# Kernel tuning notes

Measured on AMD Instinct MI355X. Metric: run time of the kernel, lower is better.

Reference implementation:

```python
import jax, jax.numpy as jnp
import numpy as np

HID = 256
IN_DIM = 256
OUT_DIM = 10
L_CYCLES = 6
H_CYCLES = 3
BATCH = 131072
LN_EPS = 1e-5


def _layernorm(v, w, b):
    mu = jnp.mean(v, axis=-1, keepdims=True)
    var = jnp.mean(jnp.square(v - mu), axis=-1, keepdims=True)
    return (v - mu) * jax.lax.rsqrt(var + LN_EPS) * w + b


def setup_inputs() -> dict:
    key = jax.random.key(0)
    ks = jax.random.split(key, 12)
    s = lambda fan_in: 1.0 / np.sqrt(fan_in)
    inp = {
        "x": jax.random.normal(ks[0], (BATCH, IN_DIM), dtype=jnp.float32),
        "W_in": jax.random.uniform(ks[1], (IN_DIM, HID), jnp.float32, -s(IN_DIM), s(IN_DIM)),
        "b_in": jnp.zeros((HID,), jnp.float32),
        "y_init": jax.random.normal(ks[2], (1, HID), dtype=jnp.float32) * 0.02,
        "W_up": jax.random.uniform(ks[3], (HID, 4 * HID), jnp.float32, -s(HID), s(HID)),
        "b_up": jnp.zeros((4 * HID,), jnp.float32),
        "W_down": jax.random.uniform(ks[4], (4 * HID, HID), jnp.float32, -s(4 * HID), s(4 * HID)),
        "b_down": jnp.zeros((HID,), jnp.float32),
        "ln_w": jnp.ones((HID,), jnp.float32),
        "ln_b": jnp.zeros((HID,), jnp.float32),
        "W_comb": jax.random.uniform(ks[5], (2 * HID, HID), jnp.float32, -s(2 * HID), s(2 * HID)),
        "b_comb": jnp.zeros((HID,), jnp.float32),
        "W_yt": jax.random.uniform(ks[6], (HID, HID), jnp.float32, -s(HID), s(HID)),
        "b_yt": jnp.zeros((HID,), jnp.float32),
        "W_head": jax.random.uniform(ks[7], (HID, OUT_DIM), jnp.float32, -s(HID), s(HID)),
        "b_head": jnp.zeros((OUT_DIM,), jnp.float32),
    }
    return inp


def reference(x, W_in, b_in, y_init, W_up, b_up, W_down, b_down, ln_w, ln_b,
              W_comb, b_comb, W_yt, b_yt, W_head, b_head):
    z = x @ W_in + b_in                      # [B, H]
    y = jnp.broadcast_to(y_init, (x.shape[0], HID))
    for _ in range(H_CYCLES):
        for _ in range(L_CYCLES):
            h = jax.nn.gelu(z @ W_up + b_up, approximate=False)
            h = h @ W_down + b_down
            z = _layernorm(z + h, ln_w, ln_b)
        combined = jnp.concatenate([z, y], axis=-1)   # [B, 2H]
        h = jax.nn.gelu(combined @ W_comb + b_comb, approximate=False)
        y = y + h @ W_yt + b_yt
    return y @ W_head + b_head
```

## Files before the change

kernel.cpp:

```cpp
#include <hip/hip_runtime.h>

typedef _Float16 h16;
typedef h16 h16x8 __attribute__((ext_vector_type(8)));
typedef float f32x4 __attribute__((ext_vector_type(4)));

#define MFMA16(a, b, c) __builtin_amdgcn_mfma_f32_16x16x32_f16(a, b, c, 0, 0, 0)

typedef __attribute__((address_space(1))) const char gconst_char;
typedef __attribute__((address_space(3))) char lds_char;
#define GL_LDS16(g, l) __builtin_amdgcn_global_load_lds((gconst_char*)(g), (lds_char*)(l), 16, 0, 0)

#define WIN_CSH   16384
#define WIN_OFF   0
#define WUP_CSH   16384
#define WUP_OFF   131072
#define WDN_CSH   16384
#define WDN_OFF   655360
#define WCOMB_CSH 32768
#define WCOMB_OFF 1179648
#define WYT_CSH   16384
#define WYT_OFF   1441792
#define WHEAD_SZ  8192
#define WHEAD_OFF 1572864
#define ZY_OFF    1581056
#define ZY_BYTES  (131072UL * 512UL * 2UL)

#define L_WUP0 0
#define L_WUP1 16384
#define L_WDN0 32768
#define L_WDN1 49152
#define L_HS   65536
#define L_ZT   86016
#define L_BUP  153600
#define L_BDN  157696
#define L_LNW  158720
#define L_LNB  159744
#define SMEM_MEGA 160768

#define C_WC0 0
#define C_WC1 32768
#define C_WY0 65536
#define C_WY1 81920
#define C_GS  98304
#define C_BC  118784
#define C_BY  119808
#define SMEM_COMB 120832

#define SMEM_HEAD 8192

__device__ __forceinline__ void stage_calls(const char* src, char* dst, int calls, int wave,
                                            int nw, int lane) {
  for (int i = wave; i < calls; i += nw)
    GL_LDS16(src + i * 1024 + lane * 16, dst + i * 1024);
}

__device__ __forceinline__ float gelu_f(float x) {
  float t = x * (1.5957691216f + 0.0713548354f * x * x);
  float e = __expf(-t);
  return x * __builtin_amdgcn_rcpf(1.0f + e);
}

__global__ void prepC_kernel(const float* __restrict__ src, h16* __restrict__ dst,
                             int Nsrc, int CSHh, int tot) {
  for (int d = blockIdx.x * 256 + threadIdx.x; d < tot; d += gridDim.x * 256) {
    int chunk = d / CSHh, r = d % CSHh;
    int frag = r >> 9, lane = (r >> 3) & 63, j = r & 7;
    int kk = frag >> 1, nt = frag & 1, q = lane >> 4, c = lane & 15;
    int k = kk * 32 + q * 8 + j;
    int n = chunk * 32 + nt * 16 + c;
    dst[d] = (h16)src[(long)k * Nsrc + n];
  }
}
__global__ void prepD_kernel(const float* __restrict__ src, h16* __restrict__ dst, int tot) {
  for (int d = blockIdx.x * 256 + threadIdx.x; d < tot; d += gridDim.x * 256) {
    int chunk = d >> 13, r = d & 8191;
    int nt = r >> 9, lane = (r >> 3) & 63, j = r & 7;
    int q = lane >> 4, c = lane & 15;
    int k = chunk * 32 + q * 8 + j;
    dst[d] = (h16)src[(long)k * 256 + nt * 16 + c];
  }
}
__global__ void prepH_kernel(const float* __restrict__ src, h16* __restrict__ dst) {
  for (int d = blockIdx.x * 256 + threadIdx.x; d < 4096; d += gridDim.x * 256) {
    int kk = d >> 9, lane = (d >> 3) & 63, j = d & 7;
    int q = lane >> 4, c = lane & 15;
    int k = kk * 32 + q * 8 + j;
    dst[d] = (h16)((c < 10) ? src[k * 10 + c] : 0.0f);
  }
}

__global__ __launch_bounds__(512) void mega_kernel(
    const float* x, h16* zy,
    const char* __restrict__ winP, const char* __restrict__ wupP, const char* __restrict__ wdnP,
    const float* __restrict__ b_in, const float* __restrict__ b_up,
    const float* __restrict__ b_down, const float* __restrict__ ln_w,
    const float* __restrict__ ln_b, const float* __restrict__ y_init, int first) {
  extern __shared__ char smem[];
  const int tid = threadIdx.x, wave = tid >> 6, lane = tid & 63;
  const int q = lane >> 4, c = lane & 15;
  const int lane16 = lane << 4;
  const long m0 = (long)blockIdx.x * 256 + wave * 32;

  float* bupL = (float*)(smem + L_BUP);
  float* bdnL = (float*)(smem + L_BDN);
  float* lnwL = (float*)(smem + L_LNW);
  float* lnbL = (float*)(smem + L_LNB);
  for (int i = tid; i < 1024; i += 512) bupL[i] = b_up[i];
  if (tid < 256) { bdnL[tid] = b_down[tid]; lnwL[tid] = ln_w[tid]; lnbL[tid] = ln_b[tid]; }

  f32x4 acc2[2][16];
  h16x8 az[2][8];
  h16* hsH = (h16*)(smem + L_HS + wave * 2560);
  h16* zth = (h16*)(smem + L_ZT + wave * 8448);
  const f32x4 vzero = {0.0f, 0.0f, 0.0f, 0.0f};

  if (first) {
#pragma unroll
    for (int rt = 0; rt < 2; ++rt)
#pragma unroll
      for (int kk = 0; kk < 8; ++kk) {
        const float* p = x + (m0 + rt * 16 + c) * 256 + kk * 32 + q * 8;
        f32x4 u0 = *(const f32x4*)p;
        f32x4 u1 = *(const f32x4*)(p + 4);
        h16x8 a;
        a[0] = (h16)u0[0]; a[1] = (h16)u0[1]; a[2] = (h16)u0[2]; a[3] = (h16)u0[3];
        a[4] = (h16)u1[0]; a[5] = (h16)u1[1]; a[6] = (h16)u1[2]; a[7] = (h16)u1[3];
        az[rt][kk] = a;
      }
#pragma unroll
    for (int rt = 0; rt < 2; ++rt)
#pragma unroll
      for (int nt = 0; nt < 16; ++nt) acc2[rt][nt] = vzero;

    stage_calls(winP, smem + L_WUP0, 16, wave, 8, lane);
    __syncthreads();
#pragma unroll
    for (int ncI = 0; ncI < 8; ++ncI) {
      if (ncI < 7)
        stage_calls(winP + (ncI + 1) * WIN_CSH, smem + (((ncI + 1) & 1) ? L_WUP1 : L_WUP0),
                    16, wave, 8, lane);
      const char* wb = smem + ((ncI & 1) ? L_WUP1 : L_WUP0);
#pragma unroll
      for (int kk = 0; kk < 8; ++kk)
#pragma unroll
        for (int nt = 0; nt < 2; ++nt) {
          h16x8 b = *(const h16x8*)(wb + ((kk * 2 + nt) << 10) + lane16);
          acc2[0][ncI * 2 + nt] = MFMA16(az[0][kk], b, acc2[0][ncI * 2 + nt]);
          acc2[1][ncI * 2 + nt] = MFMA16(az[1][kk], b, acc2[1][ncI * 2 + nt]);
        }
      __syncthreads();
    }
#pragma unroll
    for (int nt = 0; nt < 16; ++nt) {
      float bi = b_in[nt * 16 + c];
#pragma unroll
      for (int rt = 0; rt < 2; ++rt)
#pragma unroll
        for (int r = 0; r < 4; ++r) acc2[rt][nt][r] += bi;
    }
#pragma unroll
    for (int kk = 0; kk < 8; ++kk) {
      const float* p = y_init + kk * 32 + q * 8;
      f32x4 u0 = *(const f32x4*)p;
      f32x4 u1 = *(const f32x4*)(p + 4);
      h16x8 a;
      a[0] = (h16)u0[0]; a[1] = (h16)u0[1]; a[2] = (h16)u0[2]; a[3] = (h16)u0[3];
      a[4] = (h16)u1[0]; a[5] = (h16)u1[1]; a[6] = (h16)u1[2]; a[7] = (h16)u1[3];
#pragma unroll
      for (int rt = 0; rt < 2; ++rt)
        *(h16x8*)(zy + (m0 + rt * 16 + c) * 512 + 256 + kk * 32 + q * 8) = a;
    }
    stage_calls(wupP, smem + L_WUP0, 16, wave, 8, lane);
    stage_calls(wdnP, smem + L_WDN0, 16, wave, 8, lane);
  } else {
    stage_calls(wupP, smem + L_WUP0, 16, wave, 8, lane);
    stage_calls(wdnP, smem + L_WDN0, 16, wave, 8, lane);
#pragma unroll
    for (int rt = 0; rt < 2; ++rt)
#pragma unroll
      for (int kk = 0; kk < 8; ++kk)
        az[rt][kk] = *(const h16x8*)(zy + (m0 + rt * 16 + c) * 512 + kk * 32 + q * 8);
#pragma unroll
    for (int rt = 0; rt < 2; ++rt) {
#pragma unroll
      for (int kk = 0; kk < 8; ++kk)
        *(h16x8*)(zth + c * 264 + kk * 32 + q * 8) = az[rt][kk];
#pragma unroll
      for (int nt = 0; nt < 16; ++nt)
#pragma unroll
        for (int r = 0; r < 4; ++r)
          acc2[rt][nt][r] = (float)zth[(q * 4 + r) * 264 + nt * 16 + c];
    }
  }

  for (int it = 0; it < 6; ++it) {
    if (it > 0 || first) {
#pragma unroll
      for (int rt = 0; rt < 2; ++rt) {
#pragma unroll
        for (int nt = 0; nt < 16; ++nt)
#pragma unroll
          for (int r = 0; r < 4; ++r)
            zth[(q * 4 + r) * 264 + nt * 16 + c] = (h16)acc2[rt][nt][r];
#pragma unroll
        for (int kk = 0; kk < 8; ++kk)
          az[rt][kk] = *(const h16x8*)(zth + c * 264 + kk * 32 + q * 8);
      }
    }

    for (int nc = 0; nc < 32; ++nc) {
      const int tc = it * 32 + nc;
      __syncthreads();
      if (tc < 191) {
        const int nxt = (nc + 1) & 31;
        char* wu = smem + (((tc + 1) & 1) ? L_WUP1 : L_WUP0);
        char* wd = smem + (((tc + 1) & 1) ? L_WDN1 : L_WDN0);
        stage_calls(wupP + nxt * WUP_CSH, wu, 16, wave, 8, lane);
        stage_calls(wdnP + nxt * WDN_CSH, wd, 16, wave, 8, lane);
      }
      const char* wub = smem + ((tc & 1) ? L_WUP1 : L_WUP0);
      const char* wdb = smem + ((tc & 1) ? L_WDN1 : L_WDN0);

      f32x4 acc1[2][2];
      acc1[0][0] = vzero; acc1[0][1] = vzero; acc1[1][0] = vzero; acc1[1][1] = vzero;
#pragma unroll
      for (int kk = 0; kk < 8; ++kk)
#pragma unroll
        for (int nt = 0; nt < 2; ++nt) {
          h16x8 b = *(const h16x8*)(wub + ((kk * 2 + nt) << 10) + lane16);
          acc1[0][nt] = MFMA16(az[0][kk], b, acc1[0][nt]);
          acc1[1][nt] = MFMA16(az[1][kk], b, acc1[1][nt]);
        }
#pragma unroll
      for (int rt = 0; rt < 2; ++rt)
#pragma unroll
        for (int nt = 0; nt < 2; ++nt) {
          float bu = bupL[nc * 32 + nt * 16 + c];
#pragma unroll
          for (int r = 0; r < 4; ++r) {
            float g = gelu_f(acc1[rt][nt][r] + bu);
            hsH[(rt * 16 + q * 4 + r) * 40 + nt * 16 + c] = (h16)g;
          }
        }
      h16x8 ah0 = *(const h16x8*)(hsH + c * 40 + q * 8);
      h16x8 ah1 = *(const h16x8*)(hsH + (16 + c) * 40 + q * 8);
#pragma unroll
      for (int nt = 0; nt < 16; ++nt) {
        h16x8 b = *(const h16x8*)(wdb + (nt << 10) + lane16);
        acc2[0][nt] = MFMA16(ah0, b, acc2[0][nt]);
        acc2[1][nt] = MFMA16(ah1, b, acc2[1][nt]);
      }
    }

#pragma unroll
    for (int rt = 0; rt < 2; ++rt) {
      float sum[4] = {0, 0, 0, 0}, sq[4] = {0, 0, 0, 0};
#pragma unroll
      for (int nt = 0; nt < 16; ++nt) {
        float bd = bdnL[nt * 16 + c];
#pragma unroll
        for (int r = 0; r < 4; ++r) {
          float v = acc2[rt][nt][r] + bd;
          acc2[rt][nt][r] = v;
          sum[r] += v;
          sq[r] += v * v;
        }
      }
#pragma unroll
      for (int r = 0; r < 4; ++r)
#pragma unroll
        for (int m = 1; m < 16; m <<= 1) {
          sum[r] += __shfl_xor(sum[r], m, 16);
          sq[r] += __shfl_xor(sq[r], m, 16);
        }
      float mu[4], rs[4];
#pragma unroll
      for (int r = 0; r < 4; ++r) {
        mu[r] = sum[r] * (1.0f / 256.0f);
        float var = sq[r] * (1.0f / 256.0f) - mu[r] * mu[r];
        rs[r] = __builtin_amdgcn_rsqf(var + 1e-5f);
      }
#pragma unroll
      for (int nt = 0; nt < 16; ++nt) {
        float w = lnwL[nt * 16 + c], bb = lnbL[nt * 16 + c];
#pragma unroll
        for (int r = 0; r < 4; ++r)
          acc2[rt][nt][r] = (acc2[rt][nt][r] - mu[r]) * rs[r] * w + bb;
      }
    }
  }

#pragma unroll
  for (int rt = 0; rt < 2; ++rt) {
#pragma unroll
    for (int nt = 0; nt < 16; ++nt)
#pragma unroll
      for (int r = 0; r < 4; ++r)
        zth[(q * 4 + r) * 264 + nt * 16 + c] = (h16)acc2[rt][nt][r];
#pragma unroll
    for (int kk = 0; kk < 8; ++kk)
      *(h16x8*)(zy + (m0 + rt * 16 + c) * 512 + kk * 32 + q * 8) =
          *(const h16x8*)(zth + c * 264 + kk * 32 + q * 8);
  }
}

__global__ __launch_bounds__(512) void comb_kernel(
    h16* zy, const char* __restrict__ wcP, const char* __restrict__ wytP,
    const float* __restrict__ b_comb, const float* __restrict__ b_yt,
    const float* __restrict__ y_init, int first) {
  extern __shared__ char smem[];
  const int tid = threadIdx.x, wave = tid >> 6, lane = tid & 63;
  const int q = lane >> 4, c = lane & 15;
  const int lane16 = lane << 4;
  const long m0 = (long)blockIdx.x * 256 + wave * 32;

  float* bcL = (float*)(smem + C_BC);
  float* byL = (float*)(smem + C_BY);
  if (tid < 256) { bcL[tid] = b_comb[tid]; byL[tid] = b_yt[tid]; }

  f32x4 acc2[2][16];
  if (first) {
#pragma unroll
    for (int nt = 0; nt < 16; ++nt) {
      float yv = y_init[nt * 16 + c];
#pragma unroll
      for (int rt = 0; rt < 2; ++rt)
#pragma unroll
        for (int r = 0; r < 4; ++r) acc2[rt][nt][r] = yv;
    }
  } else {
    h16* zth = (h16*)(smem + wave * 8448);
#pragma unroll
    for (int rt = 0; rt < 2; ++rt) {
#pragma unroll
      for (int kk = 0; kk < 8; ++kk)
        *(h16x8*)(zth + c * 264 + kk * 32 + q * 8) =
            *(const h16x8*)(zy + (m0 + rt * 16 + c) * 512 + 256 + kk * 32 + q * 8);
#pragma unroll
      for (int nt = 0; nt < 16; ++nt)
#pragma unroll
        for (int r = 0; r < 4; ++r)
          acc2[rt][nt][r] = (float)zth[(q * 4 + r) * 264 + nt * 16 + c];
    }
  }
  __syncthreads();

  h16* gsH = (h16*)(smem + C_GS + wave * 2560);
  const f32x4 vzero = {0.0f, 0.0f, 0.0f, 0.0f};

  stage_calls(wcP, smem + C_WC0, 32, wave, 8, lane);
  stage_calls(wytP, smem + C_WY0, 16, wave, 8, lane);

  for (int nc = 0; nc < 8; ++nc) {
    __syncthreads();
    if (nc < 7) {
      int nb = (nc + 1) & 1;
      stage_calls(wcP + (nc + 1) * WCOMB_CSH, smem + (nb ? C_WC1 : C_WC0), 32, wave, 8, lane);
      stage_calls(wytP + (nc + 1) * WYT_CSH, smem + (nb ? C_WY1 : C_WY0), 16, wave, 8, lane);
    }
    const char* wcb = smem + ((nc & 1) ? C_WC1 : C_WC0);
    const char* wyb = smem + ((nc & 1) ? C_WY1 : C_WY0);

    f32x4 acc1[2][2];
    acc1[0][0] = vzero; acc1[0][1] = vzero; acc1[1][0] = vzero; acc1[1][1] = vzero;
#pragma unroll
    for (int kk = 0; kk < 16; ++kk) {
      h16x8 a0 = *(const h16x8*)(zy + (m0 + c) * 512 + kk * 32 + q * 8);
      h16x8 a1 = *(const h16x8*)(zy + (m0 + 16 + c) * 512 + kk * 32 + q * 8);
#pragma unroll
      for (int nt = 0; nt < 2; ++nt) {
        h16x8 b = *(const h16x8*)(wcb + ((kk * 2 + nt) << 10) + lane16);
        acc1[0][nt] = MFMA16(a0, b, acc1[0][nt]);
        acc1[1][nt] = MFMA16(a1, b, acc1[1][nt]);
      }
    }
#pragma unroll
    for (int rt = 0; rt < 2; ++rt)
#pragma unroll
      for (int nt = 0; nt < 2; ++nt) {
        float bc = bcL[nc * 32 + nt * 16 + c];
#pragma unroll
        for (int r = 0; r < 4; ++r) {
          float g = gelu_f(acc1[rt][nt][r] + bc);
          gsH[(rt * 16 + q * 4 + r) * 40 + nt * 16 + c] = (h16)g;
        }
      }
    h16x8 ah0 = *(const h16x8*)(gsH + c * 40 + q * 8);
    h16x8 ah1 = *(const h16x8*)(gsH + (16 + c) * 40 + q * 8);
#pragma unroll
    for (int nt = 0; nt < 16; ++nt) {
      h16x8 b = *(const h16x8*)(wyb + (nt << 10) + lane16);
      acc2[0][nt] = MFMA16(ah0, b, acc2[0][nt]);
      acc2[1][nt] = MFMA16(ah1, b, acc2[1][nt]);
    }
  }

  __syncthreads();
  h16* zth = (h16*)(smem + wave * 8448);
#pragma unroll
  for (int rt = 0; rt < 2; ++rt) {
#pragma unroll
    for (int nt = 0; nt < 16; ++nt) {
      float by = byL[nt * 16 + c];
#pragma unroll
      for (int r = 0; r < 4; ++r)
        zth[(q * 4 + r) * 264 + nt * 16 + c] = (h16)(acc2[rt][nt][r] + by);
    }
#pragma unroll
    for (int kk = 0; kk < 8; ++kk)
      *(h16x8*)(zy + (m0 + rt * 16 + c) * 512 + 256 + kk * 32 + q * 8) =
          *(const h16x8*)(zth + c * 264 + kk * 32 + q * 8);
  }
}

__global__ __launch_bounds__(256) void head_kernel(const h16* zy, const char* __restrict__ whP,
                                                   const float* __restrict__ b_head,
                                                   float* __restrict__ out) {
  extern __shared__ char smem[];
  const int tid = threadIdx.x, wave = tid >> 6, lane = tid & 63;
  const int q = lane >> 4, c = lane & 15;
  const int lane16 = lane << 4;
  const long m0 = (long)blockIdx.x * 128 + wave * 32;

  stage_calls(whP, smem, 8, wave, 4, lane);
  __syncthreads();

  f32x4 acc[2];
  const f32x4 vzero = {0.0f, 0.0f, 0.0f, 0.0f};
  acc[0] = vzero; acc[1] = vzero;
#pragma unroll
  for (int kk = 0; kk < 8; ++kk) {
    h16x8 b = *(const h16x8*)(smem + (kk << 10) + lane16);
#pragma unroll
    for (int rt = 0; rt < 2; ++rt) {
      h16x8 a = *(const h16x8*)(zy + (m0 + rt * 16 + c) * 512 + 256 + kk * 32 + q * 8);
      acc[rt] = MFMA16(a, b, acc[rt]);
    }
  }
  if (c < 10) {
    float bh = b_head[c];
#pragma unroll
    for (int rt = 0; rt < 2; ++rt)
#pragma unroll
      for (int r = 0; r < 4; ++r)
        out[(m0 + rt * 16 + q * 4 + r) * 10 + c] = acc[rt][r] + bh;
  }
}

extern "C" void kernel_launch(void* const* d_in, const int* in_sizes, int n_in, void* d_out,
                              int out_size, void* d_ws, size_t ws_size, hipStream_t stream) {
  (void)in_sizes; (void)n_in; (void)out_size;
  const float* x      = (const float*)d_in[0];
  const float* W_in   = (const float*)d_in[1];
  const float* b_in   = (const float*)d_in[2];
  const float* y_init = (const float*)d_in[3];
  const float* W_up   = (const float*)d_in[4];
  const float* b_up   = (const float*)d_in[5];
  const float* W_down = (const float*)d_in[6];
  const float* b_down = (const float*)d_in[7];
  const float* ln_w   = (const float*)d_in[8];
  const float* ln_b   = (const float*)d_in[9];
  const float* W_comb = (const float*)d_in[10];
  const float* b_comb = (const float*)d_in[11];
  const float* W_yt   = (const float*)d_in[12];
  const float* b_yt   = (const float*)d_in[13];
  const float* W_head = (const float*)d_in[14];
  const float* b_head = (const float*)d_in[15];

  char* ws = (char*)d_ws;
  h16* winP   = (h16*)(ws + WIN_OFF);
  h16* wupP   = (h16*)(ws + WUP_OFF);
  h16* wdnP   = (h16*)(ws + WDN_OFF);
  h16* wcombP = (h16*)(ws + WCOMB_OFF);
  h16* wytP   = (h16*)(ws + WYT_OFF);
  h16* wheadP = (h16*)(ws + WHEAD_OFF);
  h16* zy = (ws_size >= (size_t)ZY_OFF + ZY_BYTES) ? (h16*)(ws + ZY_OFF) : (h16*)d_in[0];

  hipFuncSetAttribute((const void*)mega_kernel, hipFuncAttributeMaxDynamicSharedMemorySize,
                      SMEM_MEGA);
  hipFuncSetAttribute((const void*)comb_kernel, hipFuncAttributeMaxDynamicSharedMemorySize,
                      SMEM_COMB);

  {
    int tot;
    tot = 8 * (WIN_CSH / 2);
    prepC_kernel<<<dim3((tot + 255) / 256), dim3(256), 0, stream>>>(W_in, winP, 256, WIN_CSH / 2, tot);
    tot = 32 * (WUP_CSH / 2);
    prepC_kernel<<<dim3((tot + 255) / 256), dim3(256), 0, stream>>>(W_up, wupP, 1024, WUP_CSH / 2, tot);
    tot = 8 * (WCOMB_CSH / 2);
    prepC_kernel<<<dim3((tot + 255) / 256), dim3(256), 0, stream>>>(W_comb, wcombP, 256, WCOMB_CSH / 2, tot);
    tot = 32 * (WDN_CSH / 2);
    prepD_kernel<<<dim3((tot + 255) / 256), dim3(256), 0, stream>>>(W_down, wdnP, tot);
    tot = 8 * (WYT_CSH / 2);
    prepD_kernel<<<dim3((tot + 255) / 256), dim3(256), 0, stream>>>(W_yt, wytP, tot);
    prepH_kernel<<<dim3(16), dim3(256), 0, stream>>>(W_head, wheadP);
  }

  for (int h = 0; h < 3; ++h) {
    mega_kernel<<<dim3(512), dim3(512), SMEM_MEGA, stream>>>(
        x, zy, (const char*)winP, (const char*)wupP, (const char*)wdnP, b_in, b_up, b_down,
        ln_w, ln_b, y_init, (h == 0) ? 1 : 0);
    comb_kernel<<<dim3(512), dim3(512), SMEM_COMB, stream>>>(
        zy, (const char*)wcombP, (const char*)wytP, b_comb, b_yt, y_init, (h == 0) ? 1 : 0);
  }
  head_kernel<<<dim3(1024), dim3(256), SMEM_HEAD, stream>>>(zy, (const char*)wheadP, b_head,
                                                            (float*)d_out);
}
```

Before: 4.658 ms.

## Shrink mega kernel LDS footprint to run two 256-thread blocks per CU

Replaces the large per-wave 264-stride transpose scratch with a small 72-stride slice reused from the per-wave hidden scratch, done in four column chunks. It also drops the LDS copy of b_up in favour of direct global loads, and changes the mega kernel to 256-thread blocks with launch bounds allowing two blocks per CU. The aim is to cut LDS from about 160KB to about 79KB so two blocks fit per CU and stalls overlap better. In exchange, weight staging is now repeated per 4-wave block, the layout conversion takes more chunked LDS round trips, and the register budget per thread is tighter.

Result: faster. 4.109 ms (-11.8%).

```diff
diff --git a/kernel.cpp b/kernel.cpp
--- a/kernel.cpp
+++ b/kernel.cpp
@@ -30,12 +30,10 @@
 #define L_WDN0 32768
 #define L_WDN1 49152
 #define L_HS   65536
-#define L_ZT   86016
-#define L_BUP  153600
-#define L_BDN  157696
-#define L_LNW  158720
-#define L_LNB  159744
-#define SMEM_MEGA 160768
+#define L_BDN  75776
+#define L_LNW  76800
+#define L_LNB  77824
+#define SMEM_MEGA 78848
 
 #define C_WC0 0
 #define C_WC1 32768
@@ -58,6 +56,47 @@
   float t = x * (1.5957691216f + 0.0713548354f * x * x);
   float e = __expf(-t);
   return x * __builtin_amdgcn_rcpf(1.0f + e);
+}
+
+__device__ __forceinline__ void d2a_rt(const f32x4* accRt, h16x8* azRt, h16* sl, int q, int c) {
+#pragma unroll
+  for (int cc = 0; cc < 4; ++cc) {
+#pragma unroll
+    for (int ntp = 0; ntp < 4; ++ntp)
+#pragma unroll
+      for (int r = 0; r < 4; ++r)
+        sl[(q * 4 + r) * 72 + ntp * 16 + c] = (h16)accRt[cc * 4 + ntp][r];
+#pragma unroll
+    for (int k2 = 0; k2 < 2; ++k2)
+      azRt[cc * 2 + k2] = *(const h16x8*)(sl + c * 72 + k2 * 32 + q * 8);
+  }
+}
+__device__ __forceinline__ void a2d_rt(const h16x8* azRt, f32x4* accRt, h16* sl, int q, int c) {
+#pragma unroll
+  for (int cc = 0; cc < 4; ++cc) {
+#pragma unroll
+    for (int k2 = 0; k2 < 2; ++k2)
+      *(h16x8*)(sl + c * 72 + k2 * 32 + q * 8) = azRt[cc * 2 + k2];
+#pragma unroll
+    for (int ntp = 0; ntp < 4; ++ntp)
+#pragma unroll
+      for (int r = 0; r < 4; ++r)
+        accRt[cc * 4 + ntp][r] = (float)sl[(q * 4 + r) * 72 + ntp * 16 + c];
+  }
+}
+__device__ __forceinline__ void d2g_rt(const f32x4* accRt, h16* sl, h16* gdst, int q, int c) {
+#pragma unroll
+  for (int cc = 0; cc < 4; ++cc) {
+#pragma unroll
+    for (int ntp = 0; ntp < 4; ++ntp)
+#pragma unroll
+      for (int r = 0; r < 4; ++r)
+        sl[(q * 4 + r) * 72 + ntp * 16 + c] = (h16)accRt[cc * 4 + ntp][r];
+#pragma unroll
+    for (int k2 = 0; k2 < 2; ++k2)
+      *(h16x8*)(gdst + (long)c * 512 + cc * 64 + k2 * 32 + q * 8) =
+          *(const h16x8*)(sl + c * 72 + k2 * 32 + q * 8);
+  }
 }
 
 __global__ void prepC_kernel(const float* __restrict__ src, h16* __restrict__ dst,
@@ -89,7 +128,7 @@
   }
 }
 
-__global__ __launch_bounds__(512) void mega_kernel(
+__global__ __launch_bounds__(256, 2) void mega_kernel(
     const float* x, h16* zy,
     const char* __restrict__ winP, const char* __restrict__ wupP, const char* __restrict__ wdnP,
     const float* __restrict__ b_in, const float* __restrict__ b_up,
@@ -99,19 +138,16 @@
   const int tid = threadIdx.x, wave = tid >> 6, lane = tid & 63;
   const int q = lane >> 4, c = lane & 15;
   const int lane16 = lane << 4;
-  const long m0 = (long)blockIdx.x * 256 + wave * 32;
-
-  float* bupL = (float*)(smem + L_BUP);
+  const long m0 = (long)blockIdx.x * 128 + wave * 32;
+
   float* bdnL = (float*)(smem + L_BDN);
   float* lnwL = (float*)(smem + L_LNW);
   float* lnbL = (float*)(smem + L_LNB);
-  for (int i = tid; i < 1024; i += 512) bupL[i] = b_up[i];
-  if (tid < 256) { bdnL[tid] = b_down[tid]; lnwL[tid] = ln_w[tid]; lnbL[tid] = ln_b[tid]; }
+  bdnL[tid] = b_down[tid]; lnwL[tid] = ln_w[tid]; lnbL[tid] = ln_b[tid];
 
   f32x4 acc2[2][16];
   h16x8 az[2][8];
   h16* hsH = (h16*)(smem + L_HS + wave * 2560);
-  h16* zth = (h16*)(smem + L_ZT + wave * 8448);
   const f32x4 vzero = {0.0f, 0.0f, 0.0f, 0.0f};
 
   if (first) {
@@ -132,13 +168,13 @@
 #pragma unroll
       for (int nt = 0; nt < 16; ++nt) acc2[rt][nt] = vzero;
 
-    stage_calls(winP, smem + L_WUP0, 16, wave, 8, lane);
+    stage_calls(winP, smem + L_WUP0, 16, wave, 4, lane);
     __syncthreads();
 #pragma unroll
     for (int ncI = 0; ncI < 8; ++ncI) {
       if (ncI < 7)
         stage_calls(winP + (ncI + 1) * WIN_CSH, smem + (((ncI + 1) & 1) ? L_WUP1 : L_WUP0),
-                    16, wave, 8, lane);
+                    16, wave, 4, lane);
       const char* wb = smem + ((ncI & 1) ? L_WUP1 : L_WUP0);
 #pragma unroll
       for (int kk = 0; kk < 8; ++kk)
@@ -170,44 +206,23 @@
       for (int rt = 0; rt < 2; ++rt)
         *(h16x8*)(zy + (m0 + rt * 16 + c) * 512 + 256 + kk * 32 + q * 8) = a;
     }
-    stage_calls(wupP, smem + L_WUP0, 16, wave, 8, lane);
-    stage_calls(wdnP, smem + L_WDN0, 16, wave, 8, lane);
+    stage_calls(wupP, smem + L_WUP0, 16, wave, 4, lane);
+    stage_calls(wdnP, smem + L_WDN0, 16, wave, 4, lane);
+#pragma unroll
+    for (int rt = 0; rt < 2; ++rt) d2a_rt(acc2[rt], az[rt], hsH, q, c);
   } else {
-    stage_calls(wupP, smem + L_WUP0, 16, wave, 8, lane);
-    stage_calls(wdnP, smem + L_WDN0, 16, wave, 8, lane);
+    stage_calls(wupP, smem + L_WUP0, 16, wave, 4, lane);
+    stage_calls(wdnP, smem + L_WDN0, 16, wave, 4, lane);
 #pragma unroll
     for (int rt = 0; rt < 2; ++rt)
 #pragma unroll
       for (int kk = 0; kk < 8; ++kk)
         az[rt][kk] = *(const h16x8*)(zy + (m0 + rt * 16 + c) * 512 + kk * 32 + q * 8);
 #pragma unroll
-    for (int rt = 0; rt < 2; ++rt) {
-#pragma unroll
-      for (int kk = 0; kk < 8; ++kk)
-        *(h16x8*)(zth + c * 264 + kk * 32 + q * 8) = az[rt][kk];
-#pragma unroll
-      for (int nt = 0; nt < 16; ++nt)
-#pragma unroll
-        for (int r = 0; r < 4; ++r)
-          acc2[rt][nt][r] = (float)zth[(q * 4 + r) * 264 + nt * 16 + c];
-    }
+    for (int rt = 0; rt < 2; ++rt) a2d_rt(az[rt], acc2[rt], hsH, q, c);
   }
 
   for (int it = 0; it < 6; ++it) {
-    if (it > 0 || first) {
-#pragma unroll
-      for (int rt = 0; rt < 2; ++rt) {
-#pragma unroll
-        for (int nt = 0; nt < 16; ++nt)
-#pragma unroll
-          for (int r = 0; r < 4; ++r)
-            zth[(q * 4 + r) * 264 + nt * 16 + c] = (h16)acc2[rt][nt][r];
-#pragma unroll
-        for (int kk = 0; kk < 8; ++kk)
-          az[rt][kk] = *(const h16x8*)(zth + c * 264 + kk * 32 + q * 8);
-      }
-    }
-
     for (int nc = 0; nc < 32; ++nc) {
       const int tc = it * 32 + nc;
       __syncthreads();
@@ -215,9 +230,11 @@
         const int nxt = (nc + 1) & 31;
         char* wu = smem + (((tc + 1) & 1) ? L_WUP1 : L_WUP0);
         char* wd = smem + (((tc + 1) & 1) ? L_WDN1 : L_WDN0);
-        stage_calls(wupP + nxt * WUP_CSH, wu, 16, wave, 8, lane);
-        stage_calls(wdnP + nxt * WDN_CSH, wd, 16, wave, 8, lane);
-      }
+        stage_calls(wupP + nxt * WUP_CSH, wu, 16, wave, 4, lane);
+        stage_calls(wdnP + nxt * WDN_CSH, wd, 16, wave, 4, lane);
+      }
+      float bu0 = b_up[nc * 32 + c];
+      float bu1 = b_up[nc * 32 + 16 + c];
       const char* wub = smem + ((tc & 1) ? L_WUP1 : L_WUP0);
       const char* wdb = smem + ((tc & 1) ? L_WDN1 : L_WDN0);
 
@@ -235,7 +252,7 @@
       for (int rt = 0; rt < 2; ++rt)
 #pragma unroll
         for (int nt = 0; nt < 2; ++nt) {
-          float bu = bupL[nc * 32 + nt * 16 + c];
+          float bu = nt ? bu1 : bu0;
 #pragma unroll
           for (int r = 0; r < 4; ++r) {
             float g = gelu_f(acc1[rt][nt][r] + bu);
@@ -287,21 +304,13 @@
         for (int r = 0; r < 4; ++r)
           acc2[rt][nt][r] = (acc2[rt][nt][r] - mu[r]) * rs[r] * w + bb;
       }
-    }
-  }
-
-#pragma unroll
-  for (int rt = 0; rt < 2; ++rt) {
-#pragma unroll
-    for (int nt = 0; nt < 16; ++nt)
-#pragma unroll
-      for (int r = 0; r < 4; ++r)
-        zth[(q * 4 + r) * 264 + nt * 16 + c] = (h16)acc2[rt][nt][r];
-#pragma unroll
-    for (int kk = 0; kk < 8; ++kk)
-      *(h16x8*)(zy + (m0 + rt * 16 + c) * 512 + kk * 32 + q * 8) =
-          *(const h16x8*)(zth + c * 264 + kk * 32 + q * 8);
-  }
+      if (it < 5) d2a_rt(acc2[rt], az[rt], hsH, q, c);
+    }
+  }
+
+#pragma unroll
+  for (int rt = 0; rt < 2; ++rt)
+    d2g_rt(acc2[rt], hsH, zy + (m0 + rt * 16) * 512, q, c);
 }
 
 __global__ __launch_bounds__(512) void comb_kernel(
@@ -318,6 +327,12 @@
   float* byL = (float*)(smem + C_BY);
   if (tid < 256) { bcL[tid] = b_comb[tid]; byL[tid] = b_yt[tid]; }
 
+  h16* gsH = (h16*)(smem + C_GS + wave * 2560);
+  const f32x4 vzero = {0.0f, 0.0f, 0.0f, 0.0f};
+
+  stage_calls(wcP, smem + C_WC0, 32, wave, 8, lane);
+  stage_calls(wytP, smem + C_WY0, 16, wave, 8, lane);
+
   f32x4 acc2[2][16];
   if (first) {
 #pragma unroll
@@ -329,27 +344,15 @@
         for (int r = 0; r < 4; ++r) acc2[rt][nt][r] = yv;
     }
   } else {
-    h16* zth = (h16*)(smem + wave * 8448);
 #pragma unroll
     for (int rt = 0; rt < 2; ++rt) {
+      h16x8 yf[8];
 #pragma unroll
       for (int kk = 0; kk < 8; ++kk)
-        *(h16x8*)(zth + c * 264 + kk * 32 + q * 8) =
-            *(const h16x8*)(zy + (m0 + rt * 16 + c) * 512 + 256 + kk * 32 + q * 8);
-#pragma unroll
-      for (int nt = 0; nt < 16; ++nt)
-#pragma unroll
-        for (int r = 0; r < 4; ++r)
-          acc2[rt][nt][r] = (float)zth[(q * 4 + r) * 264 + nt * 16 + c];
-    }
-  }
-  __syncthreads();
-
-  h16* gsH = (h16*)(smem + C_GS + wave * 2560);
-  const f32x4 vzero = {0.0f, 0.0f, 0.0f, 0.0f};
-
-  stage_calls(wcP, smem + C_WC0, 32, wave, 8, lane);
-  stage_calls(wytP, smem + C_WY0, 16, wave, 8, lane);
+        yf[kk] = *(const h16x8*)(zy + (m0 + rt * 16 + c) * 512 + 256 + kk * 32 + q * 8);
+      a2d_rt(yf, acc2[rt], gsH, q, c);
+    }
+  }
 
   for (int nc = 0; nc < 8; ++nc) {
     __syncthreads();
@@ -395,21 +398,15 @@
     }
   }
 
-  __syncthreads();
-  h16* zth = (h16*)(smem + wave * 8448);
 #pragma unroll
   for (int rt = 0; rt < 2; ++rt) {
 #pragma unroll
     for (int nt = 0; nt < 16; ++nt) {
       float by = byL[nt * 16 + c];
 #pragma unroll
-      for (int r = 0; r < 4; ++r)
-        zth[(q * 4 + r) * 264 + nt * 16 + c] = (h16)(acc2[rt][nt][r] + by);
-    }
-#pragma unroll
-    for (int kk = 0; kk < 8; ++kk)
-      *(h16x8*)(zy + (m0 + rt * 16 + c) * 512 + 256 + kk * 32 + q * 8) =
-          *(const h16x8*)(zth + c * 264 + kk * 32 + q * 8);
+      for (int r = 0; r < 4; ++r) acc2[rt][nt][r] += by;
+    }
+    d2g_rt(acc2[rt], gsH, zy + (m0 + rt * 16) * 512 + 256, q, c);
   }
 }
 
@@ -497,7 +494,7 @@
   }
 
   for (int h = 0; h < 3; ++h) {
-    mega_kernel<<<dim3(512), dim3(512), SMEM_MEGA, stream>>>(
+    mega_kernel<<<dim3(1024), dim3(256), SMEM_MEGA, stream>>>(
         x, zy, (const char*)winP, (const char*)wupP, (const char*)wdnP, b_in, b_up, b_down,
         ln_w, ln_b, y_init, (h == 0) ? 1 : 0);
     comb_kernel<<<dim3(512), dim3(512), SMEM_COMB, stream>>>(
```

## Halve rows per wave and shrink LDS to fit two blocks per CU

Applied to the files above, without the earlier changes.

Each wave now processes 16 rows instead of 32, which halves the accumulator and A-fragment register footprint. The large per-wave transpose buffer is replaced with a small shared slice, cutting LDS from about 160KB to 83KB so two 512-thread blocks can share a CU. The grid doubles to 1024 blocks, and launch_bounds(512,2) asks the compiler to cap registers accordingly. The tradeoff is that each wave gets half the reuse of every weight fragment read from LDS, so LDS traffic per MFMA doubles. The comb kernel also preloads the z/y A fragments into registers once instead of reloading them from global memory for every chunk.

Result: no change. 4.618 ms (-0.9%).

```diff
diff --git a/kernel.cpp b/kernel.cpp
--- a/kernel.cpp
+++ b/kernel.cpp
@@ -30,23 +30,24 @@
 #define L_WDN0 32768
 #define L_WDN1 49152
 #define L_HS   65536
-#define L_ZT   86016
-#define L_BUP  153600
-#define L_BDN  157696
-#define L_LNW  158720
-#define L_LNB  159744
-#define SMEM_MEGA 160768
+#define L_BUP  76288
+#define L_BDN  80384
+#define L_LNW  81408
+#define L_LNB  82432
+#define SMEM_MEGA 83456
 
 #define C_WC0 0
 #define C_WC1 32768
 #define C_WY0 65536
 #define C_WY1 81920
 #define C_GS  98304
-#define C_BC  118784
-#define C_BY  119808
-#define SMEM_COMB 120832
+#define C_BC  109056
+#define C_BY  110080
+#define SMEM_COMB 111104
 
 #define SMEM_HEAD 8192
+
+#define SLICE_W 42
 
 __device__ __forceinline__ void stage_calls(const char* src, char* dst, int calls, int wave,
                                             int nw, int lane) {
@@ -89,7 +90,7 @@
   }
 }
 
-__global__ __launch_bounds__(512) void mega_kernel(
+__global__ __launch_bounds__(512, 2) void mega_kernel(
     const float* x, h16* zy,
     const char* __restrict__ winP, const char* __restrict__ wupP, const char* __restrict__ wdnP,
     const float* __restrict__ b_in, const float* __restrict__ b_up,
@@ -99,7 +100,7 @@
   const int tid = threadIdx.x, wave = tid >> 6, lane = tid & 63;
   const int q = lane >> 4, c = lane & 15;
   const int lane16 = lane << 4;
-  const long m0 = (long)blockIdx.x * 256 + wave * 32;
+  const long m0 = (long)blockIdx.x * 128 + wave * 16;
 
   float* bupL = (float*)(smem + L_BUP);
   float* bdnL = (float*)(smem + L_BDN);
@@ -108,29 +109,24 @@
   for (int i = tid; i < 1024; i += 512) bupL[i] = b_up[i];
   if (tid < 256) { bdnL[tid] = b_down[tid]; lnwL[tid] = ln_w[tid]; lnbL[tid] = ln_b[tid]; }
 
-  f32x4 acc2[2][16];
-  h16x8 az[2][8];
-  h16* hsH = (h16*)(smem + L_HS + wave * 2560);
-  h16* zth = (h16*)(smem + L_ZT + wave * 8448);
+  f32x4 acc2[16];
+  h16x8 az[8];
+  h16* sl = (h16*)(smem + L_HS + wave * (SLICE_W * 16 * 2));
   const f32x4 vzero = {0.0f, 0.0f, 0.0f, 0.0f};
 
   if (first) {
 #pragma unroll
-    for (int rt = 0; rt < 2; ++rt)
-#pragma unroll
-      for (int kk = 0; kk < 8; ++kk) {
-        const float* p = x + (m0 + rt * 16 + c) * 256 + kk * 32 + q * 8;
-        f32x4 u0 = *(const f32x4*)p;
-        f32x4 u1 = *(const f32x4*)(p + 4);
-        h16x8 a;
-        a[0] = (h16)u0[0]; a[1] = (h16)u0[1]; a[2] = (h16)u0[2]; a[3] = (h16)u0[3];
-        a[4] = (h16)u1[0]; a[5] = (h16)u1[1]; a[6] = (h16)u1[2]; a[7] = (h16)u1[3];
-        az[rt][kk] = a;
-      }
-#pragma unroll
-    for (int rt = 0; rt < 2; ++rt)
-#pragma unroll
-      for (int nt = 0; nt < 16; ++nt) acc2[rt][nt] = vzero;
+    for (int kk = 0; kk < 8; ++kk) {
+      const float* p = x + (m0 + c) * 256 + kk * 32 + q * 8;
+      f32x4 u0 = *(const f32x4*)p;
+      f32x4 u1 = *(const f32x4*)(p + 4);
+      h16x8 a;
+      a[0] = (h16)u0[0]; a[1] = (h16)u0[1]; a[2] = (h16)u0[2]; a[3] = (h16)u0[3];
+      a[4] = (h16)u1[0]; a[5] = (h16)u1[1]; a[6] = (h16)u1[2]; a[7] = (h16)u1[3];
+      az[kk] = a;
+    }
+#pragma unroll
+    for (int nt = 0; nt < 16; ++nt) acc2[nt] = vzero;
 
     stage_calls(winP, smem + L_WUP0, 16, wave, 8, lane);
     __syncthreads();
@@ -145,8 +141,7 @@
 #pragma unroll
         for (int nt = 0; nt < 2; ++nt) {
           h16x8 b = *(const h16x8*)(wb + ((kk * 2 + nt) << 10) + lane16);
-          acc2[0][ncI * 2 + nt] = MFMA16(az[0][kk], b, acc2[0][ncI * 2 + nt]);
-          acc2[1][ncI * 2 + nt] = MFMA16(az[1][kk], b, acc2[1][ncI * 2 + nt]);
+          acc2[ncI * 2 + nt] = MFMA16(az[kk], b, acc2[ncI * 2 + nt]);
         }
       __syncthreads();
     }
@@ -154,9 +149,7 @@
     for (int nt = 0; nt < 16; ++nt) {
       float bi = b_in[nt * 16 + c];
 #pragma unroll
-      for (int rt = 0; rt < 2; ++rt)
-#pragma unroll
-        for (int r = 0; r < 4; ++r) acc2[rt][nt][r] += bi;
+      for (int r = 0; r < 4; ++r) acc2[nt][r] += bi;
     }
 #pragma unroll
     for (int kk = 0; kk < 8; ++kk) {
@@ -166,48 +159,37 @@
       h16x8 a;
       a[0] = (h16)u0[0]; a[1] = (h16)u0[1]; a[2] = (h16)u0[2]; a[3] = (h16)u0[3];
       a[4] = (h16)u1[0]; a[5] = (h16)u1[1]; a[6] = (h16)u1[2]; a[7] = (h16)u1[3];
-#pragma unroll
-      for (int rt = 0; rt < 2; ++rt)
-        *(h16x8*)(zy + (m0 + rt * 16 + c) * 512 + 256 + kk * 32 + q * 8) = a;
+      *(h16x8*)(zy + (m0 + c) * 512 + 256 + kk * 32 + q * 8) = a;
     }
     stage_calls(wupP, smem + L_WUP0, 16, wave, 8, lane);
     stage_calls(wdnP, smem + L_WDN0, 16, wave, 8, lane);
+#pragma unroll
+    for (int kk = 0; kk < 8; ++kk) {
+#pragma unroll
+      for (int n2 = 0; n2 < 2; ++n2)
+#pragma unroll
+        for (int r = 0; r < 4; ++r)
+          sl[(q * 4 + r) * SLICE_W + n2 * 16 + c] = (h16)acc2[kk * 2 + n2][r];
+      az[kk] = *(const h16x8*)(sl + c * SLICE_W + q * 8);
+    }
   } else {
     stage_calls(wupP, smem + L_WUP0, 16, wave, 8, lane);
     stage_calls(wdnP, smem + L_WDN0, 16, wave, 8, lane);
 #pragma unroll
-    for (int rt = 0; rt < 2; ++rt)
-#pragma unroll
-      for (int kk = 0; kk < 8; ++kk)
-        az[rt][kk] = *(const h16x8*)(zy + (m0 + rt * 16 + c) * 512 + kk * 32 + q * 8);
-#pragma unroll
-    for (int rt = 0; rt < 2; ++rt) {
-#pragma unroll
-      for (int kk = 0; kk < 8; ++kk)
-        *(h16x8*)(zth + c * 264 + kk * 32 + q * 8) = az[rt][kk];
-#pragma unroll
-      for (int nt = 0; nt < 16; ++nt)
+    for (int kk = 0; kk < 8; ++kk)
+      az[kk] = *(const h16x8*)(zy + (m0 + c) * 512 + kk * 32 + q * 8);
+#pragma unroll
+    for (int kk = 0; kk < 8; ++kk) {
+      *(h16x8*)(sl + c * SLICE_W + q * 8) = az[kk];
+#pragma unroll
+      for (int n2 = 0; n2 < 2; ++n2)
 #pragma unroll
         for (int r = 0; r < 4; ++r)
-          acc2[rt][nt][r] = (float)zth[(q * 4 + r) * 264 + nt * 16 + c];
+          acc2[kk * 2 + n2][r] = (float)sl[(q * 4 + r) * SLICE_W + n2 * 16 + c];
     }
   }
 
   for (int it = 0; it < 6; ++it) {
-    if (it > 0 || first) {
-#pragma unroll
-      for (int rt = 0; rt < 2; ++rt) {
-#pragma unroll
-        for (int nt = 0; nt < 16; ++nt)
-#pragma unroll
-          for (int r = 0; r < 4; ++r)
-            zth[(q * 4 + r) * 264 + nt * 16 + c] = (h16)acc2[rt][nt][r];
-#pragma unroll
-        for (int kk = 0; kk < 8; ++kk)
-          az[rt][kk] = *(const h16x8*)(zth + c * 264 + kk * 32 + q * 8);
-      }
-    }
-
     for (int nc = 0; nc < 32; ++nc) {
       const int tc = it * 32 + nc;
       __syncthreads();
@@ -221,47 +203,41 @@
       const char* wub = smem + ((tc & 1) ? L_WUP1 : L_WUP0);
       const char* wdb = smem + ((tc & 1) ? L_WDN1 : L_WDN0);
 
-      f32x4 acc1[2][2];
-      acc1[0][0] = vzero; acc1[0][1] = vzero; acc1[1][0] = vzero; acc1[1][1] = vzero;
+      f32x4 acc1[2];
+      acc1[0] = vzero; acc1[1] = vzero;
 #pragma unroll
       for (int kk = 0; kk < 8; ++kk)
 #pragma unroll
         for (int nt = 0; nt < 2; ++nt) {
           h16x8 b = *(const h16x8*)(wub + ((kk * 2 + nt) << 10) + lane16);
-          acc1[0][nt] = MFMA16(az[0][kk], b, acc1[0][nt]);
-          acc1[1][nt] = MFMA16(az[1][kk], b, acc1[1][nt]);
+          acc1[nt] = MFMA16(az[kk], b, acc1[nt]);
         }
 #pragma unroll
-      for (int rt = 0; rt < 2; ++rt)
-#pragma unroll
-        for (int nt = 0; nt < 2; ++nt) {
-          float bu = bupL[nc * 32 + nt * 16 + c];
-#pragma unroll
-          for (int r = 0; r < 4; ++r) {
-            float g = gelu_f(acc1[rt][nt][r] + bu);
-            hsH[(rt * 16 + q * 4 + r) * 40 + nt * 16 + c] = (h16)g;
-          }
+      for (int nt = 0; nt < 2; ++nt) {
+        float bu = bupL[nc * 32 + nt * 16 + c];
+#pragma unroll
+        for (int r = 0; r < 4; ++r) {
+          float g = gelu_f(acc1[nt][r] + bu);
+          sl[(q * 4 + r) * SLICE_W + nt * 16 + c] = (h16)g;
         }
-      h16x8 ah0 = *(const h16x8*)(hsH + c * 40 + q * 8);
-      h16x8 ah1 = *(const h16x8*)(hsH + (16 + c) * 40 + q * 8);
+      }
+      h16x8 ah = *(const h16x8*)(sl + c * SLICE_W + q * 8);
 #pragma unroll
       for (int nt = 0; nt < 16; ++nt) {
         h16x8 b = *(const h16x8*)(wdb + (nt << 10) + lane16);
-        acc2[0][nt] = MFMA16(ah0, b, acc2[0][nt]);
-        acc2[1][nt] = MFMA16(ah1, b, acc2[1][nt]);
-      }
-    }
-
-#pragma unroll
-    for (int rt = 0; rt < 2; ++rt) {
+        acc2[nt] = MFMA16(ah, b, acc2[nt]);
+      }
+    }
+
+    {
       float sum[4] = {0, 0, 0, 0}, sq[4] = {0, 0, 0, 0};
 #pragma unroll
       for (int nt = 0; nt < 16; ++nt) {
         float bd = bdnL[nt * 16 + c];
 #pragma unroll
         for (int r = 0; r < 4; ++r) {
-          float v = acc2[rt][nt][r] + bd;
-          acc2[rt][nt][r] = v;
+          float v = acc2[nt][r] + bd;
+          acc2[nt][r] = v;
           sum[r] += v;
           sq[r] += v * v;
         }
@@ -273,38 +249,47 @@
           sum[r] += __shfl_xor(sum[r], m, 16);
           sq[r] += __shfl_xor(sq[r], m, 16);
         }
-      float mu[4], rs[4];
 #pragma unroll
       for (int r = 0; r < 4; ++r) {
-        mu[r] = sum[r] * (1.0f / 256.0f);
-        float var = sq[r] * (1.0f / 256.0f) - mu[r] * mu[r];
-        rs[r] = __builtin_amdgcn_rsqf(var + 1e-5f);
+        float mu = sum[r] * (1.0f / 256.0f);
+        float var = sq[r] * (1.0f / 256.0f) - mu * mu;
+        float rs = __builtin_amdgcn_rsqf(var + 1e-5f);
+        sum[r] = mu; sq[r] = rs;
       }
 #pragma unroll
       for (int nt = 0; nt < 16; ++nt) {
         float w = lnwL[nt * 16 + c], bb = lnbL[nt * 16 + c];
 #pragma unroll
         for (int r = 0; r < 4; ++r)
-          acc2[rt][nt][r] = (acc2[rt][nt][r] - mu[r]) * rs[r] * w + bb;
-      }
-    }
-  }
-
-#pragma unroll
-  for (int rt = 0; rt < 2; ++rt) {
-#pragma unroll
-    for (int nt = 0; nt < 16; ++nt)
+          acc2[nt][r] = (acc2[nt][r] - sum[r]) * sq[r] * w + bb;
+      }
+    }
+    if (it < 5) {
+#pragma unroll
+      for (int kk = 0; kk < 8; ++kk) {
+#pragma unroll
+        for (int n2 = 0; n2 < 2; ++n2)
+#pragma unroll
+          for (int r = 0; r < 4; ++r)
+            sl[(q * 4 + r) * SLICE_W + n2 * 16 + c] = (h16)acc2[kk * 2 + n2][r];
+        az[kk] = *(const h16x8*)(sl + c * SLICE_W + q * 8);
+      }
+    }
+  }
+
+#pragma unroll
+  for (int kk = 0; kk < 8; ++kk) {
+#pragma unroll
+    for (int n2 = 0; n2 < 2; ++n2)
 #pragma unroll
       for (int r = 0; r < 4; ++r)
-        zth[(q * 4 + r) * 264 + nt * 16 + c] = (h16)acc2[rt][nt][r];
-#pragma unroll
-    for (int kk = 0; kk < 8; ++kk)
-      *(h16x8*)(zy + (m0 + rt * 16 + c) * 512 + kk * 32 + q * 8) =
-          *(const h16x8*)(zth + c * 264 + kk * 32 + q * 8);
-  }
-}
-
-__global__ __launch_bounds__(512) void comb_kernel(
+        sl[(q * 4 + r) * SLICE_W + n2 * 16 + c] = (h16)acc2[kk * 2 + n2][r];
+    *(h16x8*)(zy + (m0 + c) * 512 + kk * 32 + q * 8) =
+        *(const h16x8*)(sl + c * SLICE_W + q * 8);
+  }
+}
+
+__global__ __launch_bounds__(512, 2) void comb_kernel(
     h16* zy, const char* __restrict__ wcP, const char* __restrict__ wytP,
     const float* __restrict__ b_comb, const float* __restrict__ b_yt,
     const float* __restrict__ y_init, int first) {
@@ -312,44 +297,42 @@
   const int tid = threadIdx.x, wave = tid >> 6, lane = tid & 63;
   const int q = lane >> 4, c = lane & 15;
   const int lane16 = lane << 4;
-  const long m0 = (long)blockIdx.x * 256 + wave * 32;
+  const long m0 = (long)blockIdx.x * 128 + wave * 16;
 
   float* bcL = (float*)(smem + C_BC);
   float* byL = (float*)(smem + C_BY);
   if (tid < 256) { bcL[tid] = b_comb[tid]; byL[tid] = b_yt[tid]; }
 
-  f32x4 acc2[2][16];
+  h16* sl = (h16*)(smem + C_GS + wave * (SLICE_W * 16 * 2));
+  const f32x4 vzero = {0.0f, 0.0f, 0.0f, 0.0f};
+
+  stage_calls(wcP, smem + C_WC0, 32, wave, 8, lane);
+  stage_calls(wytP, smem + C_WY0, 16, wave, 8, lane);
+
+  h16x8 a[16];
+#pragma unroll
+  for (int kk = 0; kk < 16; ++kk)
+    a[kk] = *(const h16x8*)(zy + (m0 + c) * 512 + kk * 32 + q * 8);
+
+  f32x4 acc2[16];
   if (first) {
 #pragma unroll
     for (int nt = 0; nt < 16; ++nt) {
       float yv = y_init[nt * 16 + c];
 #pragma unroll
-      for (int rt = 0; rt < 2; ++rt)
-#pragma unroll
-        for (int r = 0; r < 4; ++r) acc2[rt][nt][r] = yv;
+      for (int r = 0; r < 4; ++r) acc2[nt][r] = yv;
     }
   } else {
-    h16* zth = (h16*)(smem + wave * 8448);
-#pragma unroll
-    for (int rt = 0; rt < 2; ++rt) {
-#pragma unroll
-      for (int kk = 0; kk < 8; ++kk)
-        *(h16x8*)(zth + c * 264 + kk * 32 + q * 8) =
-            *(const h16x8*)(zy + (m0 + rt * 16 + c) * 512 + 256 + kk * 32 + q * 8);
-#pragma unroll
-      for (int nt = 0; nt < 16; ++nt)
+#pragma unroll
+    for (int kk = 0; kk < 8; ++kk) {
+      *(h16x8*)(sl + c * SLICE_W + q * 8) = a[8 + kk];
+#pragma unroll
+      for (int n2 = 0; n2 < 2; ++n2)
 #pragma unroll
         for (int r = 0; r < 4; ++r)
-          acc2[rt][nt][r] = (float)zth[(q * 4 + r) * 264 + nt * 16 + c];
-    }
-  }
-  __syncthreads();
-
-  h16* gsH = (h16*)(smem + C_GS + wave * 2560);
-  const f32x4 vzero = {0.0f, 0.0f, 0.0f, 0.0f};
-
-  stage_calls(wcP, smem + C_WC0, 32, wave, 8, lane);
-  stage_calls(wytP, smem + C_WY0, 16, wave, 8, lane);
+          acc2[kk * 2 + n2][r] = (float)sl[(q * 4 + r) * SLICE_W + n2 * 16 + c];
+    }
+  }
 
   for (int nc = 0; nc < 8; ++nc) {
     __syncthreads();
@@ -361,55 +344,43 @@
     const char* wcb = smem + ((nc & 1) ? C_WC1 : C_WC0);
     const char* wyb = smem + ((nc & 1) ? C_WY1 : C_WY0);
 
-    f32x4 acc1[2][2];
-    acc1[0][0] = vzero; acc1[0][1] = vzero; acc1[1][0] = vzero; acc1[1][1] = vzero;
-#pragma unroll
-    for (int kk = 0; kk < 16; ++kk) {
-      h16x8 a0 = *(const h16x8*)(zy + (m0 + c) * 512 + kk * 32 + q * 8);
-      h16x8 a1 = *(const h16x8*)(zy + (m0 + 16 + c) * 512 + kk * 32 + q * 8);
+    f32x4 acc1[2];
+    acc1[0] = vzero; acc1[1] = vzero;
+#pragma unroll
+    for (int kk = 0; kk < 16; ++kk)
 #pragma unroll
       for (int nt = 0; nt < 2; ++nt) {
         h16x8 b = *(const h16x8*)(wcb + ((kk * 2 + nt) << 10) + lane16);
-        acc1[0][nt] = MFMA16(a0, b, acc1[0][nt]);
-        acc1[1][nt] = MFMA16(a1, b, acc1[1][nt]);
-      }
-    }
-#pragma unroll
-    for (int rt = 0; rt < 2; ++rt)
-#pragma unroll
-      for (int nt = 0; nt < 2; ++nt) {
-        float bc = bcL[nc * 32 + nt * 16 + c];
-#pragma unroll
-        for (int r = 0; r < 4; ++r) {
-          float g = gelu_f(acc1[rt][nt][r] + bc);
-          gsH[(rt * 16 + q * 4 + r) * 40 + nt * 16 + c] = (h16)g;
-        }
-      }
-    h16x8 ah0 = *(const h16x8*)(gsH + c * 40 + q * 8);
-    h16x8 ah1 = *(const h16x8*)(gsH + (16 + c) * 40 + q * 8);
+        acc1[nt] = MFMA16(a[kk], b, acc1[nt]);
+      }
+#pragma unroll
+    for (int nt = 0; nt < 2; ++nt) {
+      float bc = bcL[nc * 32 + nt * 16 + c];
+#pragma unroll
+      for (int r = 0; r < 4; ++r) {
+        float g = gelu_f(acc1[nt][r] + bc);
+        sl[(q * 4 + r) * SLICE_W + nt * 16 + c] = (h16)g;
+      }
+    }
+    h16x8 ah = *(const h16x8*)(sl + c * SLICE_W + q * 8);
 #pragma unroll
     for (int nt = 0; nt < 16; ++nt) {
       h16x8 b = *(const h16x8*)(wyb + (nt << 10) + lane16);
-      acc2[0][nt] = MFMA16(ah0, b, acc2[0][nt]);
-      acc2[1][nt] = MFMA16(ah1, b, acc2[1][nt]);
-    }
-  }
-
-  __syncthreads();
-  h16* zth = (h16*)(smem + wave * 8448);
-#pragma unroll
-  for (int rt = 0; rt < 2; ++rt) {
-#pragma unroll
-    for (int nt = 0; nt < 16; ++nt) {
-      float by = byL[nt * 16 + c];
+      acc2[nt] = MFMA16(ah, b, acc2[nt]);
+    }
+  }
+
+#pragma unroll
+  for (int kk = 0; kk < 8; ++kk) {
+#pragma unroll
+    for (int n2 = 0; n2 < 2; ++n2) {
+      float by = byL[(kk * 2 + n2) * 16 + c];
 #pragma unroll
       for (int r = 0; r < 4; ++r)
-        zth[(q * 4 + r) * 264 + nt * 16 + c] = (h16)(acc2[rt][nt][r] + by);
-    }
-#pragma unroll
-    for (int kk = 0; kk < 8; ++kk)
-      *(h16x8*)(zy + (m0 + rt * 16 + c) * 512 + 256 + kk * 32 + q * 8) =
-          *(const h16x8*)(zth + c * 264 + kk * 32 + q * 8);
+        sl[(q * 4 + r) * SLICE_W + n2 * 16 + c] = (h16)(acc2[kk * 2 + n2][r] + by);
+    }
+    *(h16x8*)(zy + (m0 + c) * 512 + 256 + kk * 32 + q * 8) =
+        *(const h16x8*)(sl + c * SLICE_W + q * 8);
   }
 }
 
@@ -497,10 +468,10 @@
   }
 
   for (int h = 0; h < 3; ++h) {
-    mega_kernel<<<dim3(512), dim3(512), SMEM_MEGA, stream>>>(
+    mega_kernel<<<dim3(1024), dim3(512), SMEM_MEGA, stream>>>(
         x, zy, (const char*)winP, (const char*)wupP, (const char*)wdnP, b_in, b_up, b_down,
         ln_w, ln_b, y_init, (h == 0) ? 1 : 0);
-    comb_kernel<<<dim3(512), dim3(512), SMEM_COMB, stream>>>(
+    comb_kernel<<<dim3(1024), dim3(512), SMEM_COMB, stream>>>(
         zy, (const char*)wcombP, (const char*)wytP, b_comb, b_yt, y_init, (h == 0) ? 1 : 0);
   }
   head_kernel<<<dim3(1024), dim3(256), SMEM_HEAD, stream>>>(zy, (const char*)wheadP, b_head,
```
